# Kernel optimization log

Hardware: AMD Instinct MI355X
Metric: run time of the kernel (lower is better)

Reference implementation:

```python
import jax, jax.numpy as jnp
import numpy as np

BETA = 0.001  # l2 regularization coefficient from __init__
N_SEG = 4096


def _pair_indices(cu):
    # Build global pair index arrays (pos<neg within each segment),
    # equivalent to torch.combinations(arange(L), 2) per segment.
    cache = {}
    pos_l, neg_l, seg_l = [], [], []
    for s in range(len(cu) - 1):
        a, b = int(cu[s]), int(cu[s + 1])
        L = b - a
        if L not in cache:
            cache[L] = np.triu_indices(L, 1)
        i, j = cache[L]
        pos_l.append(a + i)
        neg_l.append(a + j)
        seg_l.append(np.full(i.shape[0], s, dtype=np.int64))
    pos = np.concatenate(pos_l).astype(np.int64)
    neg = np.concatenate(neg_l).astype(np.int64)
    seg = np.concatenate(seg_l)
    counts = np.bincount(seg, minlength=len(cu) - 1).astype(np.float32)
    return pos, neg, seg, counts


def setup_inputs() -> dict:
    key = jax.random.key(0)
    rng = np.random.default_rng(0)
    lengths = rng.integers(32, 128, N_SEG)  # variable candidates per prompt
    cu = np.concatenate([[0], np.cumsum(lengths)]).astype(np.int64)
    n = int(cu[-1])
    logits = jax.random.normal(key, (n,), dtype=jnp.float32)
    return {"logits": logits, "cu_lengths": jnp.asarray(cu)}


def reference(logits, cu_lengths):
    cu = np.asarray(jax.device_get(cu_lengths))  # boundaries are static ints
    pos_idx, neg_idx, seg_id, counts = _pair_indices(cu)
    pos_idx = jnp.asarray(pos_idx)
    neg_idx = jnp.asarray(neg_idx)
    seg_id = jnp.asarray(seg_id)
    counts = jnp.asarray(counts)

    pos = logits[pos_idx]  # [P]
    neg = logits[neg_idx]  # [P]
    l2 = 0.5 * (pos * pos + neg * neg)
    pair_loss = -jax.nn.log_sigmoid(pos - neg) + BETA * l2  # [P]
    # per-segment mean, then mean over segments (reduction='mean')
    seg_sum = jax.ops.segment_sum(pair_loss, seg_id, num_segments=len(cu) - 1)
    per_seg = seg_sum / counts
    return jnp.mean(per_seg)
```

## Files before the change

kernel.cpp:

```cpp
#include <hip/hip_runtime.h>
#include <math.h>

#define BETA 0.001f
#define WPB  4


__device__ __forceinline__ float lane_bcast(float v, int lane_u) {
    return __uint_as_float(
        (unsigned)__builtin_amdgcn_readlane((int)__float_as_uint(v), lane_u));
}

__global__ __launch_bounds__(WPB * 64) void rmloss_part(
    const float* __restrict__ logits,
    const int*   __restrict__ cu,
    float*       __restrict__ part,
    int n_seg, float inv_n)
{
    const int wave = threadIdx.x >> 6;
    const int lane = threadIdx.x & 63;
    const int s = blockIdx.x * WPB + wave;
    if (s >= n_seg) return;

    const int a   = cu[s];
    const int L   = cu[s + 1] - a;
    const int Lm1 = L - 1;

    const float kNL2E = -1.44269504088896340736f;
    const float kT2L2 =  1.38629436111989061883f;

    const bool a_ok = lane < L;
    const bool b_ok = lane + 64 < L;
    const float va = a_ok ? logits[a + lane] : 0.0f;
    const float vb = b_ok ? logits[a + lane + 64] : 0.0f;

    float su_a = 0.0f, p_a = 1.0f;
    float su_b = 0.0f, p_b = 1.0f;

    if (L > 64) {
        #pragma unroll 4
        for (int j = 0; j < 64; ++j) {
            const float v  = lane_bcast(va, j);
            const float ua = fabsf(va - v);
            su_a += ua;
            p_a = fmaf(p_a, __builtin_amdgcn_exp2f(ua * kNL2E), p_a);
            const float ub = fabsf(vb - v);
            su_b += ub;
            p_b = fmaf(p_b, __builtin_amdgcn_exp2f(ub * kNL2E), p_b);
        }
        const int t2 = L - 64;
        #pragma unroll 4
        for (int j = 0; j < t2; ++j) {
            const float v  = lane_bcast(vb, j);
            const float ua = fabsf(va - v);
            su_a += ua;
            p_a = fmaf(p_a, __builtin_amdgcn_exp2f(ua * kNL2E), p_a);
            const float ub = fabsf(vb - v);
            su_b += ub;
            p_b = fmaf(p_b, __builtin_amdgcn_exp2f(ub * kNL2E), p_b);
        }
    } else {
        #pragma unroll 4
        for (int j = 0; j < L; ++j) {
            const float v  = lane_bcast(va, j);
            const float ua = fabsf(va - v);
            su_a += ua;
            p_a = fmaf(p_a, __builtin_amdgcn_exp2f(ua * kNL2E), p_a);
        }
    }

    const float ha = su_a + kT2L2 * __builtin_amdgcn_logf(p_a);
    const float hb = su_b + kT2L2 * __builtin_amdgcn_logf(p_b);
    const float acch = (a_ok ? ha : 0.0f) + (b_ok ? hb : 0.0f);

    const float lin = va * (float)(2 * lane - Lm1)
                    + vb * (float)(2 * (lane + 64) - Lm1);
    const float sq  = va * va + vb * vb;

    float f = 0.25f * acch + 0.5f * lin + (0.5f * BETA * (float)Lm1) * sq;
    #pragma unroll
    for (int off = 32; off > 0; off >>= 1)
        f += __shfl_down(f, off, 64);

    if (lane == 0) {
        const float P    = 0.5f * (float)(L * Lm1);
        const float diag = 0.25f * (float)L * kT2L2;
        part[s] = (f - diag) / P * inv_n;
    }
}

__global__ __launch_bounds__(256) void rmloss_reduce(
    const float* __restrict__ part, float* __restrict__ out, int n)
{
    const int t = threadIdx.x;
    float acc = 0.0f;

    const int n4 = n >> 2;
    const float4* __restrict__ p4 = (const float4*)part;
    for (int i = t; i < n4; i += 256) {
        const float4 v = p4[i];
        acc += (v.x + v.y) + (v.z + v.w);
    }
    for (int i = (n4 << 2) + t; i < n; i += 256)
        acc += part[i];

    #pragma unroll
    for (int off = 32; off > 0; off >>= 1)
        acc += __shfl_down(acc, off, 64);

    __shared__ float ws[4];
    if ((t & 63) == 0) ws[t >> 6] = acc;
    __syncthreads();
    if (t == 0) out[0] = (ws[0] + ws[1]) + (ws[2] + ws[3]);
}

extern "C" void kernel_launch(void* const* d_in, const int* in_sizes, int n_in,
                              void* d_out, int out_size, void* d_ws, size_t ws_size,
                              hipStream_t stream) {
    (void)n_in; (void)out_size; (void)ws_size;

    const float* logits = (const float*)d_in[0];
    const int*   cu     = (const int*)d_in[1];
    float*       out    = (float*)d_out;
    float*       part   = (float*)d_ws;

    const int n_seg  = in_sizes[1] - 1;
    const int blocks = (n_seg + WPB - 1) / WPB;

    rmloss_part<<<blocks, WPB * 64, 0, stream>>>(logits, cu, part, n_seg,
                                                 1.0f / (float)n_seg);
    rmloss_reduce<<<1, 256, 0, stream>>>(part, out, n_seg);
}
```

Before: 70.55 us.

## Fuse per-segment and final reduction into one cooperative kernel with grid sync

Merges the two launches into a single cooperative kernel. Each block first reduces its per-segment values in shared memory, and after a grid-wide sync block 0 sums the per-block partials. This removes the second kernel launch and shrinks the partial array fourfold. The cost is a grid barrier across 1024 blocks and the overhead of a cooperative launch, which requires every block to be co-resident.

```diff
diff --git a/kernel.cpp b/kernel.cpp
--- a/kernel.cpp
+++ b/kernel.cpp
@@ -1,5 +1,8 @@
 #include <hip/hip_runtime.h>
+#include <hip/hip_cooperative_groups.h>
 #include <math.h>
+
+namespace cg = cooperative_groups;
 
 #define BETA 0.001f
 #define WPB  4
@@ -10,107 +13,121 @@
         (unsigned)__builtin_amdgcn_readlane((int)__float_as_uint(v), lane_u));
 }
 
-__global__ __launch_bounds__(WPB * 64) void rmloss_part(
+__global__ __launch_bounds__(WPB * 64) void rmloss_coop(
     const float* __restrict__ logits,
     const int*   __restrict__ cu,
     float*       __restrict__ part,
+    float*       __restrict__ out,
     int n_seg, float inv_n)
 {
     const int wave = threadIdx.x >> 6;
     const int lane = threadIdx.x & 63;
     const int s = blockIdx.x * WPB + wave;
-    if (s >= n_seg) return;
 
-    const int a   = cu[s];
-    const int L   = cu[s + 1] - a;
-    const int Lm1 = L - 1;
+    __shared__ float wsum[WPB];
 
     const float kNL2E = -1.44269504088896340736f;
     const float kT2L2 =  1.38629436111989061883f;
 
-    const bool a_ok = lane < L;
-    const bool b_ok = lane + 64 < L;
-    const float va = a_ok ? logits[a + lane] : 0.0f;
-    const float vb = b_ok ? logits[a + lane + 64] : 0.0f;
+    float segval = 0.0f;
 
-    float su_a = 0.0f, p_a = 1.0f;
-    float su_b = 0.0f, p_b = 1.0f;
+    if (s < n_seg) {
+        const int a   = cu[s];
+        const int L   = cu[s + 1] - a;
+        const int Lm1 = L - 1;
 
-    if (L > 64) {
-        #pragma unroll 4
-        for (int j = 0; j < 64; ++j) {
-            const float v  = lane_bcast(va, j);
-            const float ua = fabsf(va - v);
-            su_a += ua;
-            p_a = fmaf(p_a, __builtin_amdgcn_exp2f(ua * kNL2E), p_a);
-            const float ub = fabsf(vb - v);
-            su_b += ub;
-            p_b = fmaf(p_b, __builtin_amdgcn_exp2f(ub * kNL2E), p_b);
+        const bool a_ok = lane < L;
+        const bool b_ok = lane + 64 < L;
+        const float va = a_ok ? logits[a + lane] : 0.0f;
+        const float vb = b_ok ? logits[a + lane + 64] : 0.0f;
+
+        float su_a = 0.0f, p_a = 1.0f;
+        float su_b = 0.0f, p_b = 1.0f;
+
+        if (L > 64) {
+            #pragma unroll 4
+            for (int j = 0; j < 64; ++j) {
+                const float v  = lane_bcast(va, j);
+                const float ua = fabsf(va - v);
+                su_a += ua;
+                p_a = fmaf(p_a, __builtin_amdgcn_exp2f(ua * kNL2E), p_a);
+                const float ub = fabsf(vb - v);
+                su_b += ub;
+                p_b = fmaf(p_b, __builtin_amdgcn_exp2f(ub * kNL2E), p_b);
+            }
+            const int t2 = L - 64;
+            #pragma unroll 4
+            for (int j = 0; j < t2; ++j) {
+                const float v  = lane_bcast(vb, j);
+                const float ua = fabsf(va - v);
+                su_a += ua;
+                p_a = fmaf(p_a, __builtin_amdgcn_exp2f(ua * kNL2E), p_a);
+                const float ub = fabsf(vb - v);
+                su_b += ub;
+                p_b = fmaf(p_b, __builtin_amdgcn_exp2f(ub * kNL2E), p_b);
+            }
+        } else {
+            #pragma unroll 4
+            for (int j = 0; j < L; ++j) {
+                const float v  = lane_bcast(va, j);
+                const float ua = fabsf(va - v);
+                su_a += ua;
+                p_a = fmaf(p_a, __builtin_amdgcn_exp2f(ua * kNL2E), p_a);
+            }
         }
-        const int t2 = L - 64;
-        #pragma unroll 4
-        for (int j = 0; j < t2; ++j) {
-            const float v  = lane_bcast(vb, j);
-            const float ua = fabsf(va - v);
-            su_a += ua;
-            p_a = fmaf(p_a, __builtin_amdgcn_exp2f(ua * kNL2E), p_a);
-            const float ub = fabsf(vb - v);
-            su_b += ub;
-            p_b = fmaf(p_b, __builtin_amdgcn_exp2f(ub * kNL2E), p_b);
-        }
-    } else {
-        #pragma unroll 4
-        for (int j = 0; j < L; ++j) {
-            const float v  = lane_bcast(va, j);
-            const float ua = fabsf(va - v);
-            su_a += ua;
-            p_a = fmaf(p_a, __builtin_amdgcn_exp2f(ua * kNL2E), p_a);
+
+        const float ha = su_a + kT2L2 * __builtin_amdgcn_logf(p_a);
+        const float hb = su_b + kT2L2 * __builtin_amdgcn_logf(p_b);
+        const float acch = (a_ok ? ha : 0.0f) + (b_ok ? hb : 0.0f);
+
+        const float lin = va * (float)(2 * lane - Lm1)
+                        + vb * (float)(2 * (lane + 64) - Lm1);
+        const float sq  = va * va + vb * vb;
+
+        float f = 0.25f * acch + 0.5f * lin + (0.5f * BETA * (float)Lm1) * sq;
+        #pragma unroll
+        for (int off = 32; off > 0; off >>= 1)
+            f += __shfl_down(f, off, 64);
+
+        if (lane == 0) {
+            const float P    = 0.5f * (float)(L * Lm1);
+            const float diag = 0.25f * (float)L * kT2L2;
+            segval = (f - diag) / P * inv_n;
         }
     }
 
-    const float ha = su_a + kT2L2 * __builtin_amdgcn_logf(p_a);
-    const float hb = su_b + kT2L2 * __builtin_amdgcn_logf(p_b);
-    const float acch = (a_ok ? ha : 0.0f) + (b_ok ? hb : 0.0f);
+    if (lane == 0) wsum[wave] = segval;
+    __syncthreads();
+    if (threadIdx.x == 0)
+        part[blockIdx.x] = (wsum[0] + wsum[1]) + (wsum[2] + wsum[3]);
 
-    const float lin = va * (float)(2 * lane - Lm1)
-                    + vb * (float)(2 * (lane + 64) - Lm1);
-    const float sq  = va * va + vb * vb;
+    __threadfence();
+    cg::this_grid().sync();
 
-    float f = 0.25f * acch + 0.5f * lin + (0.5f * BETA * (float)Lm1) * sq;
-    #pragma unroll
-    for (int off = 32; off > 0; off >>= 1)
-        f += __shfl_down(f, off, 64);
+    if (blockIdx.x == 0) {
+        __threadfence();
+        const int t    = threadIdx.x;
+        const int nblk = (int)gridDim.x;
+        float acc = 0.0f;
 
-    if (lane == 0) {
-        const float P    = 0.5f * (float)(L * Lm1);
-        const float diag = 0.25f * (float)L * kT2L2;
-        part[s] = (f - diag) / P * inv_n;
+        const int n4 = nblk >> 2;
+        const float4* __restrict__ p4 = (const float4*)part;
+        for (int i = t; i < n4; i += WPB * 64) {
+            const float4 v = p4[i];
+            acc += (v.x + v.y) + (v.z + v.w);
+        }
+        for (int i = (n4 << 2) + t; i < nblk; i += WPB * 64)
+            acc += part[i];
+
+        #pragma unroll
+        for (int off = 32; off > 0; off >>= 1)
+            acc += __shfl_down(acc, off, 64);
+
+        if (lane == 0) wsum[wave] = acc;
+        __syncthreads();
+        if (t == 0)
+            out[0] = (wsum[0] + wsum[1]) + (wsum[2] + wsum[3]);
     }
-}
-
-__global__ __launch_bounds__(256) void rmloss_reduce(
-    const float* __restrict__ part, float* __restrict__ out, int n)
-{
-    const int t = threadIdx.x;
-    float acc = 0.0f;
-
-    const int n4 = n >> 2;
-    const float4* __restrict__ p4 = (const float4*)part;
-    for (int i = t; i < n4; i += 256) {
-        const float4 v = p4[i];
-        acc += (v.x + v.y) + (v.z + v.w);
-    }
-    for (int i = (n4 << 2) + t; i < n; i += 256)
-        acc += part[i];
-
-    #pragma unroll
-    for (int off = 32; off > 0; off >>= 1)
-        acc += __shfl_down(acc, off, 64);
-
-    __shared__ float ws[4];
-    if ((t & 63) == 0) ws[t >> 6] = acc;
-    __syncthreads();
-    if (t == 0) out[0] = (ws[0] + ws[1]) + (ws[2] + ws[3]);
 }
 
 extern "C" void kernel_launch(void* const* d_in, const int* in_sizes, int n_in,
@@ -123,10 +140,12 @@
     float*       out    = (float*)d_out;
     float*       part   = (float*)d_ws;
 
-    const int n_seg  = in_sizes[1] - 1;
-    const int blocks = (n_seg + WPB - 1) / WPB;
+    int n_seg  = in_sizes[1] - 1;
+    int blocks = (n_seg + WPB - 1) / WPB;
+    float inv_n = 1.0f / (float)n_seg;
 
-    rmloss_part<<<blocks, WPB * 64, 0, stream>>>(logits, cu, part, n_seg,
-                                                 1.0f / (float)n_seg);
-    rmloss_reduce<<<1, 256, 0, stream>>>(part, out, n_seg);
+    void* args[] = { (void*)&logits, (void*)&cu, (void*)&part, (void*)&out,
+                     (void*)&n_seg, (void*)&inv_n };
+    hipLaunchCooperativeKernel((void*)rmloss_coop, dim3(blocks),
+                               dim3(WPB * 64), args, 0, stream);
 }
```

New measurement: 177.3 us. 151% more time.
